# Performance work log

Measured on AMD Instinct MI355X. Metric: run time of the kernel, lower is better.

The kernel has to match this reference:

```python
import jax, jax.numpy as jnp
import numpy as np

B, C, T, V, H = 64, 256, 64, 25, 512


def setup_inputs() -> dict:
    key = jax.random.key(0)
    k_h, k_w1, k_w2, k_r = jax.random.split(key, 4)
    h = jax.random.normal(k_h, (B, C, T, V), dtype=jnp.float32)
    W1 = jax.random.normal(k_w1, (C, H), dtype=jnp.float32) * 0.02
    b1 = jnp.zeros((H,), dtype=jnp.float32)
    W2 = jax.random.normal(k_w2, (H, C), dtype=jnp.float32) * 0.02
    b2 = jnp.zeros((C,), dtype=jnp.float32)
    # per-step teacher-forcing uniforms, one per (timestep, batch elem)
    tf_rand = jax.random.uniform(k_r, (T - 1, B), dtype=jnp.float32)
    return {"h": h, "W1": W1, "b1": b1, "W2": W2, "b2": b2,
            "tf_rand": tf_rand, "t_obs": 16}


def reference(h, W1, b1, W2, b2, tf_rand, t_obs):
    # training=True, run_backwards=False branch of ODEEulerSolver.forward
    # ode_func: 2-layer MLP over the channel dim (time index unused)
    def ode(z):  # z: [B, C, V]
        u = jnp.tanh(jnp.einsum('bcv,ch->bhv', z, W1) + b1[None, :, None])
        return jnp.einsum('bhv,hc->bcv', u, W2) + b2[None, :, None]

    z0 = h[:, :, 0, :]                           # [B, C, V]
    h_prev = jnp.moveaxis(h[:, :, :-1, :], 2, 0)  # [T-1, B, C, V] teacher states

    def step(z_prev, inp):
        h_t, r = inp                              # h_t: [B,C,V], r: [B]
        # rand < 0.5 -> keep previous prediction, else teacher-force h[:, :, t-1]
        mask = (r < 0.5)[:, None, None]
        z_t = jnp.where(mask, z_prev, h_t)
        z_next = z_t + ode(z_t)                   # Euler step
        return z_next, z_next

    _, zs = jax.lax.scan(step, z0, (h_prev, tf_rand))  # zs: [T-1, B, C, V]
    z_hat = jnp.concatenate([z0[:, :, None, :], jnp.moveaxis(zs, 0, 2)], axis=2)
    return z_hat  # [B, C, T, V]
```

## Files before the change

### kernel.cpp

```cpp
#include <hip/hip_runtime.h>
#include <hip/hip_bf16.h>
#include <math.h>


using bf16x8 = __attribute__((ext_vector_type(8))) short;
using f32x4  = __attribute__((ext_vector_type(4))) float;

constexpr int Bb = 64, Cc = 256, Tt = 64, Vv = 25, Hh = 512;
constexpr int TV = Tt * Vv;
constexpr int MAXCH = Bb * (Tt - 1);
constexpr int NGRID = 2496;
constexpr int NTMAX = 4;

__device__ __forceinline__ short f2bf(float x) {
  union { float f; unsigned u; } v; v.f = x;
  unsigned r = v.u + 0x7FFFu + ((v.u >> 16) & 1u);
  return (short)(r >> 16);
}
__device__ __forceinline__ float fast_tanh(float x) {
  float e = __expf(2.f * x);
  return 1.f - 2.f * __builtin_amdgcn_rcpf(e + 1.f);
}
__device__ __forceinline__ void bar_lds() {
  asm volatile("s_waitcnt lgkmcnt(0)" ::: "memory");
  __builtin_amdgcn_s_barrier();
  asm volatile("" ::: "memory");
}
__device__ __forceinline__ void gl2lds16(const short* g, short* l) {
  __builtin_amdgcn_global_load_lds(
      (const __attribute__((address_space(1))) void*)g,
      (__attribute__((address_space(3))) void*)l, 16, 0, 0);
}

__global__ void prep_kernel(const float* __restrict__ W1,
                            const float* __restrict__ W2,
                            const float* __restrict__ tf,
                            short* __restrict__ a1p,
                            short* __restrict__ a2p,
                            int* __restrict__ sorted,
                            int* __restrict__ hdr) {
  if (blockIdx.x < 1024) {
    int idx = blockIdx.x * 256 + threadIdx.x;
    if (idx < 131072) {
      int j = idx & 7, lane = (idx >> 3) & 63, mt = (idx >> 9) & 31, kt = idx >> 14;
      int h = mt * 16 + (lane & 15);
      int c = kt * 32 + (lane >> 4) * 8 + j;
      a1p[idx] = f2bf(W1[c * Hh + h]);
    } else {
      int i2 = idx - 131072;
      int j = i2 & 7, lane = (i2 >> 3) & 63, mt = (i2 >> 9) & 15, kt = i2 >> 13;
      int cm = mt * 16 + (lane & 15);
      int hk = kt * 32 + (lane >> 4) * 8 + j;
      a2p[i2] = f2bf(W2[hk * Cc + cm]);
    }
    return;
  }
  __shared__ int cnt[64];
  __shared__ int ofs[64];
  int tid = threadIdx.x;
  if (tid < 64) cnt[tid] = 0;
  for (int i = tid; i < MAXCH; i += 256) sorted[i] = 0;
  __syncthreads();
  if (tid < Bb) {
    int b = tid, prev = 0;
    for (int t = 1; t <= 62; t++)
      if (tf[t * Bb + b] >= 0.5f) { atomicAdd(&cnt[t - prev], 1); prev = t; }
    atomicAdd(&cnt[63 - prev], 1);
  }
  __syncthreads();
  if (tid == 0) {
    int acc = 0;
    for (int l = 63; l >= 1; l--) { ofs[l] = acc; acc += cnt[l]; }
    int n1 = 0;
    for (int l = 5; l <= 63; l++) n1 += cnt[l];
    hdr[0] = n1;
    hdr[1] = (acc - n1 + 1) >> 1;
    hdr[2] = acc; hdr[3] = 0;
  }
  __syncthreads();
  if (tid < Bb) {
    int b = tid, prev = 0;
    for (int t = 1; t <= 62; t++) {
      if (tf[t * Bb + b] >= 0.5f) {
        int len = t - prev;
        int p = atomicAdd(&ofs[len], 1);
        sorted[p] = b | (prev << 6) | (len << 12);
        prev = t;
      }
    }
    int len = 63 - prev;
    int p = atomicAdd(&ofs[len], 1);
    sorted[p] = b | (prev << 6) | (len << 12);
  }
}

template<int NCH>
__device__ __forceinline__ void run_group(
    int start,
    const float* __restrict__ hsrc, const float* __restrict__ b1,
    const float* __restrict__ b2,   const short* __restrict__ a1p,
    const short* __restrict__ a2p,  const int* __restrict__ sorted,
    float* __restrict__ out, short* __restrict__ zB, short* __restrict__ uB,
    short* __restrict__ wA) {
  constexpr int NTA = NCH * 2;
  const int tid  = threadIdx.x;
  const int lane = tid & 63;
  const int w    = tid >> 6;
  const int m16  = lane & 15;
  const int quad = lane >> 4;
  short* wv = wA + w * 4096;

  int meta[NCH], len[NCH], sbase[NCH], t0s[NCH];
  #pragma unroll
  for (int j = 0; j < NCH; j++) {
    meta[j]  = sorted[start + j];
    len[j]   = (meta[j] >> 12) & 63;
    t0s[j]   = (meta[j] >> 6) & 63;
    sbase[j] = (meta[j] & 63) * Cc * TV + t0s[j] * Vv;
  }
  const int maxlen = len[0];

  f32x4 acc2[2][NTA];

  #pragma unroll
  for (int i = 0; i < 2; i++) {
    const int cbase = (w * 2 + i) * 16 + quad * 4;
    const int ktz = cbase >> 5;
    const int gq  = (cbase >> 3) & 3;
    const int j0  = cbase & 7;
    #pragma unroll
    for (int nt = 0; nt < NTA; nt++) {
      const int j  = nt >> 1;
      const int v  = (nt & 1) * 16 + m16;
      const bool valid = (len[j] > 0) && (v < Vv);
      const int hb = sbase[j] + cbase * TV + v;
      f32x4 z;
      #pragma unroll
      for (int r = 0; r < 4; r++)
        z[r] = valid ? __builtin_nontemporal_load(&hsrc[hb + r * TV]) : 0.f;
      acc2[i][nt] = z;
      short4 zh;
      zh.x = f2bf(z[0]); zh.y = f2bf(z[1]); zh.z = f2bf(z[2]); zh.w = f2bf(z[3]);
      *(short4*)&zB[((ktz * NTMAX + nt) * 64 + m16 + 16 * gq) * 8 + j0] = zh;
      if (valid && t0s[j] == 0) {
        #pragma unroll
        for (int r = 0; r < 4; r++) out[hb + r * TV] = z[r];
      }
    }
  }

  auto ISSUE = [&](int tile) {
    const int kt = tile & 7;
    const short* gp;
    switch (tile >> 3) {
      case 0:  gp = a1p + ((kt * 32 +      w * 2) * 64 + lane) * 8; break;
      case 1:  gp = a2p + (((     kt) * 16 + w * 2) * 64 + lane) * 8; break;
      case 2:  gp = a1p + ((kt * 32 + 16 + w * 2) * 64 + lane) * 8; break;
      default: gp = a2p + (((8 +  kt) * 16 + w * 2) * 64 + lane) * 8; break;
    }
    short* lp = wv + (tile & 3) * 1024;
    gl2lds16(gp, lp);
    gl2lds16(gp + 512, lp + 512);
  };

  ISSUE(0);
  ISSUE(1);
  bar_lds();

  f32x4 b2v[2];
  #pragma unroll
  for (int i = 0; i < 2; i++) {
    const float4 t = *(const float4*)(b2 + (w * 2 + i) * 16 + quad * 4);
    b2v[i] = (f32x4){t.x, t.y, t.z, t.w};
  }

  for (int s = 0; s < maxlen; s++) {
    auto MMPH = [&](int ph, f32x4 (&acc)[2][NTA], const short* Bp, bool relax) {
      #pragma unroll
      for (int kt = 0; kt < 8; kt++) {
        const int tile = ph * 8 + kt;
        ISSUE((tile + 2) & 31);
        if (relax && kt == 0)      asm volatile("s_waitcnt vmcnt(18)" ::: "memory");
        else if (relax && kt == 1) asm volatile("s_waitcnt vmcnt(20)" ::: "memory");
        else                       asm volatile("s_waitcnt vmcnt(4)"  ::: "memory");
        const short* wp = wv + (tile & 3) * 1024 + lane * 8;
        bf16x8 af0 = *(const bf16x8*)wp;
        bf16x8 af1 = *(const bf16x8*)(wp + 512);
        #pragma unroll
        for (int nt = 0; nt < NTA; nt++) {
          bf16x8 bb = *(const bf16x8*)&Bp[((kt * NTMAX + nt) * 64 + lane) * 8];
          acc[0][nt] = __builtin_amdgcn_mfma_f32_16x16x32_bf16(af0, bb, acc[0][nt], 0, 0, 0);
          acc[1][nt] = __builtin_amdgcn_mfma_f32_16x16x32_bf16(af1, bb, acc[1][nt], 0, 0, 0);
        }
      }
    };
    auto UEPI = [&](int chunk, f32x4 (&a1)[2][NTA]) {
      #pragma unroll
      for (int i = 0; i < 2; i++) {
        const int hl  = (w * 2 + i) * 16 + quad * 4;
        const int ktl = hl >> 5;
        const int gq  = (hl >> 3) & 3;
        const int j0  = hl & 7;
        const float4 b1v = *(const float4*)(b1 + chunk * 256 + hl);
        #pragma unroll
        for (int nt = 0; nt < NTA; nt++) {
          short4 up;
          up.x = f2bf(fast_tanh(a1[i][nt][0] + b1v.x));
          up.y = f2bf(fast_tanh(a1[i][nt][1] + b1v.y));
          up.z = f2bf(fast_tanh(a1[i][nt][2] + b1v.z));
          up.w = f2bf(fast_tanh(a1[i][nt][3] + b1v.w));
          *(short4*)&uB[((ktl * NTMAX + nt) * 64 + m16 + 16 * gq) * 8 + j0] = up;
        }
      }
    };

    #pragma unroll
    for (int i = 0; i < 2; i++)
      #pragma unroll
      for (int nt = 0; nt < NTA; nt++) {
        acc2[i][nt][0] += b2v[i][0]; acc2[i][nt][1] += b2v[i][1];
        acc2[i][nt][2] += b2v[i][2]; acc2[i][nt][3] += b2v[i][3];
      }

    f32x4 acc1[2][NTA];
    #pragma unroll
    for (int i = 0; i < 2; i++)
      #pragma unroll
      for (int nt = 0; nt < NTA; nt++) acc1[i][nt] = (f32x4){0.f, 0.f, 0.f, 0.f};
    MMPH(0, acc1, zB, s > 0);
    UEPI(0, acc1);
    bar_lds();
    MMPH(1, acc2, uB, false);
    #pragma unroll
    for (int i = 0; i < 2; i++)
      #pragma unroll
      for (int nt = 0; nt < NTA; nt++) acc1[i][nt] = (f32x4){0.f, 0.f, 0.f, 0.f};
    MMPH(2, acc1, zB, false);
    bar_lds();
    UEPI(1, acc1);
    bar_lds();
    MMPH(3, acc2, uB, false);
    #pragma unroll
    for (int i = 0; i < 2; i++) {
      const int cbase = (w * 2 + i) * 16 + quad * 4;
      const int ktz = cbase >> 5;
      const int gq  = (cbase >> 3) & 3;
      const int j0  = cbase & 7;
      #pragma unroll
      for (int nt = 0; nt < NTA; nt++) {
        short4 zh;
        zh.x = f2bf(acc2[i][nt][0]); zh.y = f2bf(acc2[i][nt][1]);
        zh.z = f2bf(acc2[i][nt][2]); zh.w = f2bf(acc2[i][nt][3]);
        *(short4*)&zB[((ktz * NTMAX + nt) * 64 + m16 + 16 * gq) * 8 + j0] = zh;
        const int v = (nt & 1) * 16 + m16;
        if (v < Vv && s < len[nt >> 1]) {
          const int o = sbase[nt >> 1] + cbase * TV + v + (s + 1) * Vv;
          out[o]          = acc2[i][nt][0];
          out[o + TV]     = acc2[i][nt][1];
          out[o + 2 * TV] = acc2[i][nt][2];
          out[o + 3 * TV] = acc2[i][nt][3];
        }
      }
    }
    bar_lds();
  }
}

__global__ __launch_bounds__(512, 1) void group_kernel(
    const float* __restrict__ hsrc, const float* __restrict__ b1,
    const float* __restrict__ b2,   const short* __restrict__ a1p,
    const short* __restrict__ a2p,  const int* __restrict__ sorted,
    const int* __restrict__ hdr,    float* __restrict__ out) {
  __shared__ __align__(16) short zB[8 * NTMAX * 64 * 8];
  __shared__ __align__(16) short uB[8 * NTMAX * 64 * 8];
  __shared__ __align__(16) short wA[8 * 4 * 1024];

  const int n1 = hdr[0], npair = hdr[1];
  const int bi = blockIdx.x;
  if (bi < n1) {
    run_group<1>(bi, hsrc, b1, b2, a1p, a2p, sorted, out, zB, uB, wA);
  } else if (bi < n1 + npair) {
    run_group<2>(n1 + (bi - n1) * 2, hsrc, b1, b2, a1p, a2p, sorted, out, zB, uB, wA);
  }
}

extern "C" void kernel_launch(void* const* d_in, const int* in_sizes, int n_in,
                              void* d_out, int out_size, void* d_ws, size_t ws_size,
                              hipStream_t stream) {
  const float* h_ptr = (const float*)d_in[0];
  const float* W1    = (const float*)d_in[1];
  const float* b1    = (const float*)d_in[2];
  const float* W2    = (const float*)d_in[3];
  const float* b2    = (const float*)d_in[4];
  const float* tf    = (const float*)d_in[5];
  float* out = (float*)d_out;

  short* a1p  = (short*)d_ws;
  short* a2p  = a1p + 131072;
  int* sorted = (int*)(a2p + 131072);
  int* hdr    = sorted + MAXCH;

  prep_kernel<<<1025, 256, 0, stream>>>(W1, W2, tf, a1p, a2p, sorted, hdr);
  group_kernel<<<NGRID, 512, 0, stream>>>(h_ptr, b1, b2, a1p, a2p, sorted, hdr, out);
}
```

Before: 353.2 us.

## Keep W1 fragments resident in registers and stream only W2 through LDS

Each wave loads its slice of W1 (both hidden chunks, all k-tiles) into registers once before the time loop. The first matmul then reads weights from registers instead of re-streaming them through LDS every step, and the async LDS pipeline now cycles over 16 W2 tiles instead of 32. b1 is also hoisted into registers, and launch bounds change to request two blocks per CU. The W1 fragments take 64 VGPRs per lane, so the register cap from the occupancy-2 bound could force spills or starve the MFMA accumulators.

```diff
diff --git a/kernel.cpp b/kernel.cpp
--- a/kernel.cpp
+++ b/kernel.cpp
@@ -120,6 +120,16 @@
   }
   const int maxlen = len[0];
 
+  bf16x8 w1r[2][8][2];
+  #pragma unroll
+  for (int ch = 0; ch < 2; ch++)
+    #pragma unroll
+    for (int kt = 0; kt < 8; kt++) {
+      const short* ab = a1p + ((kt * 32 + ch * 16 + w * 2) * 64 + lane) * 8;
+      w1r[ch][kt][0] = *(const bf16x8*)ab;
+      w1r[ch][kt][1] = *(const bf16x8*)(ab + 512);
+    }
+
   f32x4 acc2[2][NTA];
 
   #pragma unroll
@@ -150,14 +160,7 @@
   }
 
   auto ISSUE = [&](int tile) {
-    const int kt = tile & 7;
-    const short* gp;
-    switch (tile >> 3) {
-      case 0:  gp = a1p + ((kt * 32 +      w * 2) * 64 + lane) * 8; break;
-      case 1:  gp = a2p + (((     kt) * 16 + w * 2) * 64 + lane) * 8; break;
-      case 2:  gp = a1p + ((kt * 32 + 16 + w * 2) * 64 + lane) * 8; break;
-      default: gp = a2p + (((8 +  kt) * 16 + w * 2) * 64 + lane) * 8; break;
-    }
+    const short* gp = a2p + ((tile * 16 + w * 2) * 64 + lane) * 8;
     short* lp = wv + (tile & 3) * 1024;
     gl2lds16(gp, lp);
     gl2lds16(gp + 512, lp + 512);
@@ -168,47 +171,61 @@
   bar_lds();
 
   f32x4 b2v[2];
+  f32x4 b1v[2][2];
   #pragma unroll
   for (int i = 0; i < 2; i++) {
     const float4 t = *(const float4*)(b2 + (w * 2 + i) * 16 + quad * 4);
     b2v[i] = (f32x4){t.x, t.y, t.z, t.w};
+    #pragma unroll
+    for (int ch = 0; ch < 2; ch++) {
+      const float4 u = *(const float4*)(b1 + ch * 256 + (w * 2 + i) * 16 + quad * 4);
+      b1v[ch][i] = (f32x4){u.x, u.y, u.z, u.w};
+    }
   }
 
   for (int s = 0; s < maxlen; s++) {
-    auto MMPH = [&](int ph, f32x4 (&acc)[2][NTA], const short* Bp, bool relax) {
+    auto MM1R = [&](int ch, f32x4 (&a1)[2][NTA]) {
       #pragma unroll
       for (int kt = 0; kt < 8; kt++) {
-        const int tile = ph * 8 + kt;
-        ISSUE((tile + 2) & 31);
-        if (relax && kt == 0)      asm volatile("s_waitcnt vmcnt(18)" ::: "memory");
-        else if (relax && kt == 1) asm volatile("s_waitcnt vmcnt(20)" ::: "memory");
-        else                       asm volatile("s_waitcnt vmcnt(4)"  ::: "memory");
+        #pragma unroll
+        for (int nt = 0; nt < NTA; nt++) {
+          bf16x8 bz = *(const bf16x8*)&zB[((kt * NTMAX + nt) * 64 + lane) * 8];
+          a1[0][nt] = __builtin_amdgcn_mfma_f32_16x16x32_bf16(w1r[ch][kt][0], bz, a1[0][nt], 0, 0, 0);
+          a1[1][nt] = __builtin_amdgcn_mfma_f32_16x16x32_bf16(w1r[ch][kt][1], bz, a1[1][nt], 0, 0, 0);
+        }
+      }
+    };
+    auto MM2R = [&](int ch) {
+      #pragma unroll
+      for (int kt = 0; kt < 8; kt++) {
+        const int tile = ch * 8 + kt;
+        ISSUE((tile + 2) & 15);
+        asm volatile("s_waitcnt vmcnt(4)" ::: "memory");
         const short* wp = wv + (tile & 3) * 1024 + lane * 8;
         bf16x8 af0 = *(const bf16x8*)wp;
         bf16x8 af1 = *(const bf16x8*)(wp + 512);
         #pragma unroll
         for (int nt = 0; nt < NTA; nt++) {
-          bf16x8 bb = *(const bf16x8*)&Bp[((kt * NTMAX + nt) * 64 + lane) * 8];
-          acc[0][nt] = __builtin_amdgcn_mfma_f32_16x16x32_bf16(af0, bb, acc[0][nt], 0, 0, 0);
-          acc[1][nt] = __builtin_amdgcn_mfma_f32_16x16x32_bf16(af1, bb, acc[1][nt], 0, 0, 0);
+          bf16x8 bu = *(const bf16x8*)&uB[((kt * NTMAX + nt) * 64 + lane) * 8];
+          acc2[0][nt] = __builtin_amdgcn_mfma_f32_16x16x32_bf16(af0, bu, acc2[0][nt], 0, 0, 0);
+          acc2[1][nt] = __builtin_amdgcn_mfma_f32_16x16x32_bf16(af1, bu, acc2[1][nt], 0, 0, 0);
         }
       }
     };
-    auto UEPI = [&](int chunk, f32x4 (&a1)[2][NTA]) {
+    auto UEPI = [&](int ch, f32x4 (&a1)[2][NTA]) {
       #pragma unroll
       for (int i = 0; i < 2; i++) {
         const int hl  = (w * 2 + i) * 16 + quad * 4;
         const int ktl = hl >> 5;
         const int gq  = (hl >> 3) & 3;
         const int j0  = hl & 7;
-        const float4 b1v = *(const float4*)(b1 + chunk * 256 + hl);
         #pragma unroll
         for (int nt = 0; nt < NTA; nt++) {
           short4 up;
-          up.x = f2bf(fast_tanh(a1[i][nt][0] + b1v.x));
-          up.y = f2bf(fast_tanh(a1[i][nt][1] + b1v.y));
-          up.z = f2bf(fast_tanh(a1[i][nt][2] + b1v.z));
-          up.w = f2bf(fast_tanh(a1[i][nt][3] + b1v.w));
+          up.x = f2bf(fast_tanh(a1[i][nt][0] + b1v[ch][i][0]));
+          up.y = f2bf(fast_tanh(a1[i][nt][1] + b1v[ch][i][1]));
+          up.z = f2bf(fast_tanh(a1[i][nt][2] + b1v[ch][i][2]));
+          up.w = f2bf(fast_tanh(a1[i][nt][3] + b1v[ch][i][3]));
           *(short4*)&uB[((ktl * NTMAX + nt) * 64 + m16 + 16 * gq) * 8 + j0] = up;
         }
       }
@@ -227,19 +244,19 @@
     for (int i = 0; i < 2; i++)
       #pragma unroll
       for (int nt = 0; nt < NTA; nt++) acc1[i][nt] = (f32x4){0.f, 0.f, 0.f, 0.f};
-    MMPH(0, acc1, zB, s > 0);
+    MM1R(0, acc1);
     UEPI(0, acc1);
     bar_lds();
-    MMPH(1, acc2, uB, false);
+    MM2R(0);
     #pragma unroll
     for (int i = 0; i < 2; i++)
       #pragma unroll
       for (int nt = 0; nt < NTA; nt++) acc1[i][nt] = (f32x4){0.f, 0.f, 0.f, 0.f};
-    MMPH(2, acc1, zB, false);
+    MM1R(1, acc1);
     bar_lds();
     UEPI(1, acc1);
     bar_lds();
-    MMPH(3, acc2, uB, false);
+    MM2R(1);
     #pragma unroll
     for (int i = 0; i < 2; i++) {
       const int cbase = (w * 2 + i) * 16 + quad * 4;
@@ -266,7 +283,7 @@
   }
 }
 
-__global__ __launch_bounds__(512, 1) void group_kernel(
+__global__ __launch_bounds__(512, 2) void group_kernel(
     const float* __restrict__ hsrc, const float* __restrict__ b1,
     const float* __restrict__ b2,   const short* __restrict__ a1p,
     const short* __restrict__ a2p,  const int* __restrict__ sorted,
```

After: 440.0 us. 24.6% more time.
